# Performance work log

Hardware: AMD Instinct MI355X
Metric: run time of the kernel (lower is better)

Reference implementation:

```python
import jax, jax.numpy as jnp
import numpy as np

T, B, F_, H, D, C = 16, 1024, 512, 128, 8, 100  # trees, batch, feat, hidden, depth, classes
L = 2 ** (D + 1)  # n_leaf = 512


def _routing_tables():
    # Static per-leaf routing: node index and branch side at each depth.
    # Derived from compute_mu's gather indices:
    #   node(d, l) = 2^d - 1 + l // 2^(D+1-d);  side(d, l) = (l // 2^(D-d)) % 2
    l = np.arange(L)
    node = np.stack([(2 ** d - 1) + l // (2 ** (D + 1 - d)) for d in range(D + 1)])  # [D+1, L]
    side = np.stack([(l // (2 ** (D - d))) % 2 for d in range(D + 1)])               # [D+1, L]
    return jnp.asarray(node, dtype=jnp.int32), jnp.asarray(side.astype(np.bool_))


def setup_inputs() -> dict:
    key = jax.random.key(0)
    ks = jax.random.split(key, 4)
    return {
        "feat": jax.random.normal(ks[0], (B, F_), jnp.float32),
        "W1": jax.random.normal(ks[1], (T, F_, H), jnp.float32) * 0.05,
        "b1": jnp.zeros((T, H), jnp.float32),
        "W2": jax.random.normal(ks[2], (T, H, L), jnp.float32) * 0.05,
        "b2": jnp.zeros((T, L), jnp.float32),
        "pi": jax.random.uniform(ks[3], (T, L, C), jnp.float32, -2.0, 2.0),
    }


def reference(feat, W1, b1, W2, b2, pi):
    node, side = _routing_tables()
    # Per-tree MLP head (dropout is identity in eval mode).
    h = jax.nn.relu(jnp.einsum('bf,tfh->tbh', feat, W1) + b1[:, None, :])        # [T,B,H]
    p = jax.nn.sigmoid(jnp.einsum('tbh,thl->tbl', h, W2) + b2[:, None, :])       # [T,B,L]
    # compute_mu: product of routing probs along each root->leaf path.
    sel = p[:, :, node]                          # [T,B,D+1,L] gather (static indices)
    route = jnp.where(side, 1.0 - sel, sel)      # left -> p, right -> 1-p
    mu = jnp.prod(route, axis=2)                 # [T,B,L]
    # compute_py_x: mean over leaves then mean over trees of mu @ softmax(pi).
    leaf_p = jax.nn.softmax(pi, axis=-1)         # [T,L,C]
    py_x = jnp.einsum('tbl,tlc->bc', mu, leaf_p) / (L * T)  # [B,C]
    return jnp.log(py_x)
```

## Files before the change

### kernel.cpp

```cpp
#include <hip/hip_runtime.h>
#include <hip/hip_bf16.h>
#include <math.h>

#define T_ 16
#define B_ 1024
#define F_ 512
#define H_ 128
#define D_ 8
#define C_ 100
#define L_ 512
#define CP_ 112

typedef __attribute__((ext_vector_type(8))) short bf16x8_t;
typedef __attribute__((ext_vector_type(4))) float f32x4_t;

__device__ inline ushort f2bf(float x) {
  __hip_bfloat16 b = __float2bfloat16(x);
  return *(ushort*)&b;
}
__device__ inline float bf2f(ushort u) {
  union { unsigned int i; float f; } v;
  v.i = ((unsigned int)u) << 16;
  return v.f;
}

__device__ inline void bar_raw() {
  asm volatile("" ::: "memory");
  __builtin_amdgcn_s_barrier();
  asm volatile("" ::: "memory");
}
__device__ inline void bar_publish_lds() {
  asm volatile("s_waitcnt lgkmcnt(0)" ::: "memory");
  __builtin_amdgcn_s_barrier();
  asm volatile("" ::: "memory");
}

__global__ __launch_bounds__(256) void k_prep(
    const float* __restrict__ W1, const float* __restrict__ W2,
    const float* __restrict__ pi, ushort* __restrict__ W1T,
    ushort* __restrict__ W2T, ushort* __restrict__ lpT) {
  __shared__ ushort ubuf[112 * 48];
  float (*tile)[33] = (float(*)[33])ubuf;
  ushort (*tileT)[48] = (ushort(*)[48])ubuf;
  const int bid = blockIdx.x, tid = threadIdx.x;

  if (bid < 2048) {
    const float* X; ushort* XT; int K, N, kb, nb, s;
    if (bid < 1024) {
      int r = bid;         kb = r & 15; nb = (r >> 4) & 3;  s = r >> 6;
      X = W1; XT = W1T; K = F_; N = H_;
    } else {
      int r = bid - 1024;  kb = r & 3;  nb = (r >> 2) & 15; s = r >> 6;
      X = W2; XT = W2T; K = H_; N = L_;
    }
    const int k0 = kb * 32, n0 = nb * 32;
    const int c = tid & 31, r0 = tid >> 5;
    const float* Xs = X + (size_t)s * K * N;
    ushort* XTs = XT + (size_t)s * N * K;
#pragma unroll
    for (int j = 0; j < 4; ++j)
      tile[r0 + 8 * j][c] = Xs[(size_t)(k0 + r0 + 8 * j) * N + n0 + c];
    __syncthreads();
#pragma unroll
    for (int j = 0; j < 4; ++j)
      XTs[(size_t)(n0 + r0 + 8 * j) * K + k0 + c] = f2bf(tile[c][r0 + 8 * j]);
    return;
  }
  {
    int bid2 = bid - 2048;
    int t = bid2 >> 4, l0 = (bid2 & 15) << 5;
    int lane = tid & 63;
#pragma unroll
    for (int p = 0; p < 8; ++p) {
      int rl = p * 4 + (tid >> 6);
      const float* x = pi + (size_t)(t * L_ + l0 + rl) * C_;
      float v0 = (lane < C_) ? x[lane] : -1e30f;
      float v1 = (lane + 64 < C_) ? x[lane + 64] : -1e30f;
      float m = fmaxf(v0, v1);
#pragma unroll
      for (int off = 32; off; off >>= 1) m = fmaxf(m, __shfl_xor(m, off, 64));
      float e0 = __expf(v0 - m);
      float e1 = (lane + 64 < C_) ? __expf(v1 - m) : 0.0f;
      float sm = e0 + e1;
#pragma unroll
      for (int off = 32; off; off >>= 1) sm += __shfl_xor(sm, off, 64);
      float inv = 1.0f / sm;
      if (lane < C_) tileT[lane][rl] = f2bf(e0 * inv);
      int c2 = lane + 64;
      if (c2 < CP_) tileT[c2][rl] = f2bf(c2 < C_ ? e1 * inv : 0.0f);
    }
    __syncthreads();
    ushort* dst = lpT + (size_t)t * CP_ * L_ + l0;
    for (int idx = tid; idx < 448; idx += 256) {
      int c = idx >> 2, ch = (idx & 3) * 8;
      *(bf16x8_t*)(dst + (size_t)c * L_ + ch) = *(const bf16x8_t*)&tileT[c][ch];
    }
  }
}

__global__ __launch_bounds__(512, 4) void k12_mfma(
    const float* __restrict__ feat, const ushort* __restrict__ W1T,
    const float* __restrict__ b1, const ushort* __restrict__ W2T,
    const float* __restrict__ b2, const ushort* __restrict__ lpT,
    float* __restrict__ part) {
  __shared__ ushort smem[38400];
  ushort (*h_s)[136] = (ushort(*)[136])smem;
  ushort (*a_s0)[72] = (ushort(*)[72])(smem + 4352);
  ushort (*a_s1)[72] = (ushort(*)[72])(smem + 4352 + 2304);
  ushort (*b_s0)[72] = (ushort(*)[72])(smem + 8960);
  ushort (*b_s1)[72] = (ushort(*)[72])(smem + 8960 + 9216);
  ushort (*w_s0)[136] = (ushort(*)[136])(smem + 4352);
  ushort (*w_s1)[136] = (ushort(*)[136])(smem + 4352 + 8704);
  ushort (*p_s)[520] = (ushort(*)[520])(smem + 21760);

  const int bid = blockIdx.x;
  const int t = bid & 15, b0 = (bid >> 4) * 32;
  const int tid = threadIdx.x;
  const int w = tid >> 6, lane = tid & 63, quad = lane >> 4, n = lane & 15;

  {
    const bool doA = tid < 256;
    const int srow = tid >> 3, scol = (tid & 7) * 8;
    const float*  fp32p = feat + (size_t)(b0 + srow) * F_ + scol;
    const ushort* w1p   = W1T + ((size_t)t * H_ + srow) * F_ + scol;

    float4 ra[2][2];
    bf16x8_t rb[2][2];

    if (doA) { ra[0][0] = *(const float4*)(fp32p);
               ra[0][1] = *(const float4*)(fp32p + 4); }
#pragma unroll
    for (int i = 0; i < 2; ++i)
      rb[0][i] = *(const bf16x8_t*)(w1p + (size_t)i * 64 * F_);
    if (doA) {
      bf16x8_t o;
      o[0] = (short)f2bf(ra[0][0].x); o[1] = (short)f2bf(ra[0][0].y);
      o[2] = (short)f2bf(ra[0][0].z); o[3] = (short)f2bf(ra[0][0].w);
      o[4] = (short)f2bf(ra[0][1].x); o[5] = (short)f2bf(ra[0][1].y);
      o[6] = (short)f2bf(ra[0][1].z); o[7] = (short)f2bf(ra[0][1].w);
      *(bf16x8_t*)&a_s0[srow][scol] = o;
    }
#pragma unroll
    for (int i = 0; i < 2; ++i)
      *(bf16x8_t*)&b_s0[i * 64 + srow][scol] = rb[0][i];
    bar_publish_lds();
    if (doA) { ra[1][0] = *(const float4*)(fp32p + 64);
               ra[1][1] = *(const float4*)(fp32p + 68); }
#pragma unroll
    for (int i = 0; i < 2; ++i)
      rb[1][i] = *(const bf16x8_t*)(w1p + (size_t)i * 64 * F_ + 64);
    if (doA) { ra[0][0] = *(const float4*)(fp32p + 128);
               ra[0][1] = *(const float4*)(fp32p + 132); }
#pragma unroll
    for (int i = 0; i < 2; ++i)
      rb[0][i] = *(const bf16x8_t*)(w1p + (size_t)i * 64 * F_ + 128);

    f32x4_t acc[2];
    acc[0] = (f32x4_t){0.f, 0.f, 0.f, 0.f};
    acc[1] = (f32x4_t){0.f, 0.f, 0.f, 0.f};
#pragma unroll
    for (int kc = 0; kc < 8; ++kc) {
      ushort (*ar)[72] = (kc & 1) ? a_s1 : a_s0;
      ushort (*br)[72] = (kc & 1) ? b_s1 : b_s0;
#pragma unroll
      for (int ks2 = 0; ks2 < 2; ++ks2) {
        const int ko = ks2 * 32 + quad * 8;
        bf16x8_t af0 = *(const bf16x8_t*)&ar[n][ko];
        bf16x8_t af1 = *(const bf16x8_t*)&ar[16 + n][ko];
        bf16x8_t bfr = *(const bf16x8_t*)&br[w * 16 + n][ko];
        acc[0] = __builtin_amdgcn_mfma_f32_16x16x32_bf16(af0, bfr, acc[0],
                                                         0, 0, 0);
        acc[1] = __builtin_amdgcn_mfma_f32_16x16x32_bf16(af1, bfr, acc[1],
                                                         0, 0, 0);
      }
      if (kc < 7) {
        const int p = (kc + 1) & 1;
        ushort (*aw)[72] = p ? a_s1 : a_s0;
        ushort (*bw)[72] = p ? b_s1 : b_s0;
        if (doA) {
          bf16x8_t o;
          o[0] = (short)f2bf(ra[p][0].x); o[1] = (short)f2bf(ra[p][0].y);
          o[2] = (short)f2bf(ra[p][0].z); o[3] = (short)f2bf(ra[p][0].w);
          o[4] = (short)f2bf(ra[p][1].x); o[5] = (short)f2bf(ra[p][1].y);
          o[6] = (short)f2bf(ra[p][1].z); o[7] = (short)f2bf(ra[p][1].w);
          *(bf16x8_t*)&aw[srow][scol] = o;
        }
#pragma unroll
        for (int i = 0; i < 2; ++i)
          *(bf16x8_t*)&bw[i * 64 + srow][scol] = rb[p][i];
        bar_publish_lds();
        if (kc < 6) {
          if (doA) { ra[p][0] = *(const float4*)(fp32p + (kc + 3) * 64);
                     ra[p][1] = *(const float4*)(fp32p + (kc + 3) * 64 + 4); }
#pragma unroll
          for (int i = 0; i < 2; ++i)
            rb[p][i] = *(const bf16x8_t*)(w1p + (size_t)i * 64 * F_ + (kc + 3) * 64);
        }
      }
    }
    float bias = b1[t * H_ + w * 16 + n];
#pragma unroll
    for (int mt = 0; mt < 2; ++mt)
#pragma unroll
      for (int r = 0; r < 4; ++r) {
        float v = acc[mt][r] + bias;
        h_s[mt * 16 + quad * 4 + r][w * 16 + n] = f2bf(v > 0.f ? v : 0.f);
      }
  }

  {
    const int wrow = tid >> 4, wcol = (tid & 15) * 8;
    const ushort* w2p = W2T + ((size_t)t * L_ + wrow) * H_ + wcol;
    bf16x8_t rw[2][2];
#pragma unroll
    for (int i = 0; i < 2; ++i)
      rw[0][i] = *(const bf16x8_t*)(w2p + (size_t)(i * 32) * H_);
#pragma unroll
    for (int i = 0; i < 2; ++i)
      rw[1][i] = *(const bf16x8_t*)(w2p + (size_t)(64 + i * 32) * H_);
    bar_publish_lds();

    const int mhalf = w >> 2, lhalf = w & 3;
    bf16x8_t af2[4];
#pragma unroll
    for (int ks = 0; ks < 4; ++ks)
      af2[ks] = *(const bf16x8_t*)&h_s[mhalf * 16 + n][ks * 32 + quad * 8];
#pragma unroll
    for (int i = 0; i < 2; ++i)
      *(bf16x8_t*)&w_s0[i * 32 + wrow][wcol] = rw[0][i];
    bar_publish_lds();
#pragma unroll
    for (int i = 0; i < 2; ++i)
      rw[0][i] = *(const bf16x8_t*)(w2p + (size_t)(128 + i * 32) * H_);

#pragma unroll
    for (int nc = 0; nc < 8; ++nc) {
      ushort (*wr)[136] = (nc & 1) ? w_s1 : w_s0;
      f32x4_t acc = (f32x4_t){0.f, 0.f, 0.f, 0.f};
#pragma unroll
      for (int ks = 0; ks < 4; ++ks) {
        bf16x8_t bfrag = *(const bf16x8_t*)&wr[lhalf * 16 + n][ks * 32 + quad * 8];
        acc = __builtin_amdgcn_mfma_f32_16x16x32_bf16(af2[ks], bfrag, acc,
                                                      0, 0, 0);
      }
      int l = nc * 64 + lhalf * 16 + n;
      float bias = b2[t * L_ + l];
#pragma unroll
      for (int r = 0; r < 4; ++r) {
        float x = acc[r] + bias;
        p_s[mhalf * 16 + quad * 4 + r][l] = f2bf(1.0f / (1.0f + __expf(-x)));
      }
      if (nc < 7) {
        const int p = (nc + 1) & 1;
        ushort (*ww)[136] = p ? w_s1 : w_s0;
#pragma unroll
        for (int i = 0; i < 2; ++i)
          *(bf16x8_t*)&ww[i * 32 + wrow][wcol] = rw[p][i];
        bar_publish_lds();
        if (nc < 6) {
#pragma unroll
          for (int i = 0; i < 2; ++i)
            rw[p][i] = *(const bf16x8_t*)(w2p + (size_t)((nc + 3) * 64 + i * 32) * H_);
        }
      }
    }
  }
  bar_publish_lds();

  bf16x8_t mo[2][2];
#pragma unroll
  for (int pass = 0; pass < 2; ++pass) {
    int unit = pass * 512 + tid;
    int b = unit >> 5;
    int s = unit & 31;
    float P = 1.f;
#pragma unroll
    for (int d = 0; d < 5; ++d) {
      int nd = (1 << d) - 1 + (s >> (5 - d));
      int sd = (s >> (4 - d)) & 1;
      float pv = bf2f(p_s[b][nd]);
      P *= sd ? (1.f - pv) : pv;
    }
    float p5 = bf2f(p_s[b][31 + s]);
    float q5[2] = {P * p5, P * (1.f - p5)};
    float q6[4], q7[8];
#pragma unroll
    for (int j = 0; j < 2; ++j) {
      float pv = bf2f(p_s[b][63 + 2 * s + j]);
      q6[2 * j] = q5[j] * pv;
      q6[2 * j + 1] = q5[j] * (1.f - pv);
    }
#pragma unroll
    for (int u = 0; u < 4; ++u) {
      float pv = bf2f(p_s[b][127 + 4 * s + u]);
      q7[2 * u] = q6[u] * pv;
      q7[2 * u + 1] = q6[u] * (1.f - pv);
    }
    bf16x8_t o0, o1;
#pragma unroll
    for (int v = 0; v < 8; ++v) {
      float pv = bf2f(p_s[b][255 + 8 * s + v]);
      ushort e0 = f2bf(q7[v] * pv);
      ushort e1 = f2bf(q7[v] * (1.f - pv));
      if (v < 4) { o0[2 * v] = (short)e0; o0[2 * v + 1] = (short)e1; }
      else       { o1[2 * (v - 4)] = (short)e0; o1[2 * (v - 4) + 1] = (short)e1; }
    }
    mo[pass][0] = o0;
    mo[pass][1] = o1;
  }
  bar_raw();
#pragma unroll
  for (int pass = 0; pass < 2; ++pass) {
    int unit = pass * 512 + tid;
    int b = unit >> 5;
    int s = unit & 31;
    *(bf16x8_t*)&p_s[b][s * 16]     = mo[pass][0];
    *(bf16x8_t*)&p_s[b][s * 16 + 8] = mo[pass][1];
  }
  bar_publish_lds();

  {
#pragma unroll
    for (int uu = 0; uu < 2; ++uu) {
      int u = w + uu * 8;
      if (u < 14) {
        const int mt = u & 1, nt = u >> 1;
        const ushort* arow = &p_s[mt * 16 + n][0];
        const ushort* brow = lpT + (size_t)t * CP_ * L_ +
                             ((size_t)(nt * 16 + n)) * L_ + quad * 8;
        f32x4_t acc = (f32x4_t){0.f, 0.f, 0.f, 0.f};
#pragma unroll 4
        for (int k = 0; k < L_; k += 32) {
          bf16x8_t af = *(const bf16x8_t*)(arow + k + quad * 8);
          bf16x8_t bfr = *(const bf16x8_t*)(brow + k);
          acc = __builtin_amdgcn_mfma_f32_16x16x32_bf16(af, bfr, acc, 0, 0, 0);
        }
        const int m0 = b0 + mt * 16 + quad * 4;
        const int c = nt * 16 + n;
        if (c < C_) {
#pragma unroll
          for (int r = 0; r < 4; ++r)
            part[((size_t)t * B_ + m0 + r) * C_ + c] = acc[r];
        }
      }
    }
  }
}

__global__ __launch_bounds__(256) void k6_log(
    const float* __restrict__ part, float* __restrict__ out) {
  int i = (blockIdx.x * 256 + threadIdx.x) * 4;
  if (i < B_ * C_) {
    float4 s = {0.f, 0.f, 0.f, 0.f};
#pragma unroll
    for (int t = 0; t < T_; ++t) {
      float4 v = *(const float4*)(part + (size_t)t * B_ * C_ + i);
      s.x += v.x; s.y += v.y; s.z += v.z; s.w += v.w;
    }
    const float inv = 1.0f / (L_ * T_);
    float4 o;
    o.x = logf(s.x * inv); o.y = logf(s.y * inv);
    o.z = logf(s.z * inv); o.w = logf(s.w * inv);
    *(float4*)(out + i) = o;
  }
}

extern "C" void kernel_launch(void* const* d_in, const int* in_sizes, int n_in,
                              void* d_out, int out_size, void* d_ws,
                              size_t ws_size, hipStream_t stream) {
  const float* feat = (const float*)d_in[0];
  const float* W1   = (const float*)d_in[1];
  const float* b1   = (const float*)d_in[2];
  const float* W2   = (const float*)d_in[3];
  const float* b2   = (const float*)d_in[4];
  const float* pi   = (const float*)d_in[5];
  float* out = (float*)d_out;

  char* ws = (char*)d_ws;
  ushort* W1T_buf  = (ushort*)(ws);
  ushort* W2T_buf  = (ushort*)(ws + ((size_t)2 << 20));
  ushort* lpT_buf  = (ushort*)(ws + ((size_t)4 << 20));
  float*  part_buf = (float*)(ws + ((size_t)6 << 20));

  k_prep<<<2304, 256, 0, stream>>>(W1, W2, pi, W1T_buf, W2T_buf, lpT_buf);
  k12_mfma<<<512, 512, 0, stream>>>(feat, W1T_buf, b1, W2T_buf, b2,
                                    lpT_buf, part_buf);
  k6_log<<<(B_ * C_ / 4 + 255) / 256, 256, 0, stream>>>(part_buf, out);
}
```

Baseline: 108.5 us.

## Fuse tree reduction and log into main kernel via atomics and last-block counter

Each block now atomically adds its per-tree partial results into a shared [B,C] accumulator instead of writing per-tree partials. A per-batch-tile counter detects the last of the 16 tree blocks, and that block applies the log and scaling, so the separate reduction kernel is removed. This saves a kernel launch and the 6.5MB partial buffer round trip. In exchange it adds a memset, float atomic contention (16 adders per element), and a summation order that is no longer deterministic.

New measurement: 127.2 us. 1.17x slower.

```diff
diff --git a/kernel.cpp b/kernel.cpp
--- a/kernel.cpp
+++ b/kernel.cpp
@@ -102,7 +102,8 @@
     const float* __restrict__ feat, const ushort* __restrict__ W1T,
     const float* __restrict__ b1, const ushort* __restrict__ W2T,
     const float* __restrict__ b2, const ushort* __restrict__ lpT,
-    float* __restrict__ part) {
+    float* __restrict__ acc_out, unsigned int* __restrict__ cnt,
+    float* __restrict__ out) {
   __shared__ ushort smem[38400];
   ushort (*h_s)[136] = (ushort(*)[136])smem;
   ushort (*a_s0)[72] = (ushort(*)[72])(smem + 4352);
@@ -112,6 +113,7 @@
   ushort (*w_s0)[136] = (ushort(*)[136])(smem + 4352);
   ushort (*w_s1)[136] = (ushort(*)[136])(smem + 4352 + 8704);
   ushort (*p_s)[520] = (ushort(*)[520])(smem + 21760);
+  __shared__ unsigned int last_flag;
 
   const int bid = blockIdx.x;
   const int t = bid & 15, b0 = (bid >> 4) * 32;
@@ -340,28 +342,29 @@
         if (c < C_) {
 #pragma unroll
           for (int r = 0; r < 4; ++r)
-            part[((size_t)t * B_ + m0 + r) * C_ + c] = acc[r];
-        }
-      }
-    }
-  }
-}
-
-__global__ __launch_bounds__(256) void k6_log(
-    const float* __restrict__ part, float* __restrict__ out) {
-  int i = (blockIdx.x * 256 + threadIdx.x) * 4;
-  if (i < B_ * C_) {
-    float4 s = {0.f, 0.f, 0.f, 0.f};
-#pragma unroll
-    for (int t = 0; t < T_; ++t) {
-      float4 v = *(const float4*)(part + (size_t)t * B_ * C_ + i);
-      s.x += v.x; s.y += v.y; s.z += v.z; s.w += v.w;
-    }
+            atomicAdd(&acc_out[(size_t)(m0 + r) * C_ + c], acc[r]);
+        }
+      }
+    }
+  }
+
+  __syncthreads();
+  if (tid == 0) {
+    __threadfence();
+    unsigned int old = __hip_atomic_fetch_add(&cnt[bid >> 4], 1u,
+                                              __ATOMIC_ACQ_REL,
+                                              __HIP_MEMORY_SCOPE_AGENT);
+    last_flag = (old == 15u) ? 1u : 0u;
+  }
+  __syncthreads();
+  if (last_flag) {
     const float inv = 1.0f / (L_ * T_);
-    float4 o;
-    o.x = logf(s.x * inv); o.y = logf(s.y * inv);
-    o.z = logf(s.z * inv); o.w = logf(s.w * inv);
-    *(float4*)(out + i) = o;
+    for (int idx = tid; idx < 32 * C_; idx += 512) {
+      size_t gi = (size_t)b0 * C_ + idx;
+      float s = __hip_atomic_load(&acc_out[gi], __ATOMIC_RELAXED,
+                                  __HIP_MEMORY_SCOPE_AGENT);
+      out[gi] = logf(s * inv);
+    }
   }
 }
 
@@ -380,10 +383,13 @@
   ushort* W1T_buf  = (ushort*)(ws);
   ushort* W2T_buf  = (ushort*)(ws + ((size_t)2 << 20));
   ushort* lpT_buf  = (ushort*)(ws + ((size_t)4 << 20));
-  float*  part_buf = (float*)(ws + ((size_t)6 << 20));
+  float*  acc_buf  = (float*)(ws + ((size_t)6 << 20));
+  unsigned int* cnt_buf =
+      (unsigned int*)(ws + ((size_t)6 << 20) + 409600);
+
+  hipMemsetAsync(acc_buf, 0, 409600 + 128, stream);
 
   k_prep<<<2304, 256, 0, stream>>>(W1, W2, pi, W1T_buf, W2T_buf, lpT_buf);
   k12_mfma<<<512, 512, 0, stream>>>(feat, W1T_buf, b1, W2T_buf, b2,
-                                    lpT_buf, part_buf);
-  k6_log<<<(B_ * C_ / 4 + 255) / 256, 256, 0, stream>>>(part_buf, out);
-}
+                                    lpT_buf, acc_buf, cnt_buf, out);
+}
```
